# Kernel tuning notes

Measured on AMD Instinct MI355X. Metric: run time of the kernel, lower is better.

## Reference

```python
import jax, jax.numpy as jnp
import numpy as np


def setup_inputs() -> dict:
    key = jax.random.key(0)
    k1, k2 = jax.random.split(key)
    lut = jax.random.normal(k1, (1, 3, 33, 33, 33), dtype=jnp.float32)
    x = jax.random.uniform(k2, (8, 3, 1024, 1024), dtype=jnp.float32)
    return {"lut": lut, "x": x}


def reference(lut, x):
    # lut: [1, 3, D, D, D]; x: [B, 3, H, W] in [0,1]
    D = lut.shape[-1]
    lut0 = lut[0]  # [3, D, D, D], broadcast over batch (lut batch == 1)

    v = jnp.clip(x, 0.0, 1.0) * (D - 1)            # [B, 3, H, W]
    v = jnp.transpose(v, (0, 2, 3, 1))             # [B, H, W, 3]
    i0 = jnp.floor(v).astype(jnp.int32)            # [B, H, W, 3]
    i1 = jnp.minimum(i0 + 1, D - 1)
    f = v - i0.astype(v.dtype)                     # fractional part

    r0, g0, b0 = i0[..., 0], i0[..., 1], i0[..., 2]
    r1, g1, b1 = i1[..., 0], i1[..., 1], i1[..., 2]
    fr, fg, fb = f[..., 0], f[..., 1], f[..., 2]

    def gather(rr, gg, bb):
        # lut0[:, rr, gg, bb] -> [3, B, H, W] -> [B, 3, H, W]
        return jnp.transpose(lut0[:, rr, gg, bb], (1, 0, 2, 3))

    c000 = gather(r0, g0, b0)
    c100 = gather(r1, g0, b0)
    c010 = gather(r0, g1, b0)
    c110 = gather(r1, g1, b0)
    c001 = gather(r0, g0, b1)
    c101 = gather(r1, g0, b1)
    c011 = gather(r0, g1, b1)
    c111 = gather(r1, g1, b1)

    one = jnp.float32(1.0)
    w000 = ((one - fr) * (one - fg) * (one - fb))[:, None]
    w100 = (fr * (one - fg) * (one - fb))[:, None]
    w010 = ((one - fr) * fg * (one - fb))[:, None]
    w110 = (fr * fg * (one - fb))[:, None]
    w001 = ((one - fr) * (one - fg) * fb)[:, None]
    w101 = (fr * (one - fg) * fb)[:, None]
    w011 = ((one - fr) * fg * fb)[:, None]
    w111 = (fr * fg * fb)[:, None]

    out = (c000 * w000 + c100 * w100 + c010 * w010 + c110 * w110 +
           c001 * w001 + c101 * w101 + c011 * w011 + c111 * w111)
    return out  # [B, 3, H, W]
```

## Files before the change

### kernel.cpp

```cpp
#include <hip/hip_runtime.h>
#include <hip/hip_fp16.h>


#define D   33
#define D2  (33 * 33)
#define D3  (33 * 33 * 33)
#define HW  (1024 * 1024)
#define BATCH 8
#define QHW (HW / 4)
#define NG  (BATCH * QHW)
#define CHUNKS 256
#define GPC (NG / CHUNKS)
#define THREADS 1024

typedef float v4f __attribute__((ext_vector_type(4)));

__global__ __launch_bounds__(THREADS) void lut3d_kernel(
    const float* __restrict__ lut, const float* __restrict__ x,
    float* __restrict__ out)
{
    const int id    = blockIdx.x;
    const int xcd   = id & 7;
    const int slot  = id >> 3;
    const int c     = slot % 3;
    const int chunk = (slot / 3) * 8 + xcd;

    __shared__ __half2 ls[D3];
    {
        const float* lc = lut + c * D3;
        for (int i = threadIdx.x; i < D3; i += THREADS) {
            const int q  = i / D;
            const int b  = i - q * D;
            const float v0 = lc[i];
            const float v1 = (b < D - 1) ? lc[i + 1] : v0;
            ls[i] = __floats2half2_rn(v0, v1);
        }
    }
    __syncthreads();

    const int tid  = threadIdx.x;
    const int base = chunk * GPC;

    #pragma unroll 1
    for (int it = 0; it < GPC / THREADS; ++it) {
        const int g = base + it * THREADS + tid;
        const int b = g >> 18;
        const int p = (g & (QHW - 1)) * 4;

        const float* xb = x + (size_t)b * 3 * HW + p;
        const v4f xr = *(const v4f*)(xb);
        const v4f xg = *(const v4f*)(xb + HW);
        const v4f xB = *(const v4f*)(xb + 2 * HW);

        v4f oo;

        #pragma unroll
        for (int j = 0; j < 4; ++j) {
            const float vr = fminf(fmaxf(xr[j], 0.f), 1.f) * 32.f;
            const float vg = fminf(fmaxf(xg[j], 0.f), 1.f) * 32.f;
            const float vb = fminf(fmaxf(xB[j], 0.f), 1.f) * 32.f;

            const int r0 = min((int)vr, D - 2);
            const int g0 = min((int)vg, D - 2);
            const int b0 = min((int)vb, D - 2);
            const float fr = vr - (float)r0;
            const float fg = vg - (float)g0;
            const float fb = vb - (float)b0;

            const int idx = r0 * D2 + g0 * D + b0;

            const __half2 h00 = ls[idx];
            const __half2 h01 = ls[idx + D];
            const __half2 h10 = ls[idx + D2];
            const __half2 h11 = ls[idx + D2 + D];

            const float c00 = fmaf(fb, __high2float(h00) - __low2float(h00), __low2float(h00));
            const float c01 = fmaf(fb, __high2float(h01) - __low2float(h01), __low2float(h01));
            const float c10 = fmaf(fb, __high2float(h10) - __low2float(h10), __low2float(h10));
            const float c11 = fmaf(fb, __high2float(h11) - __low2float(h11), __low2float(h11));

            const float c0 = fmaf(fg, c01 - c00, c00);
            const float c1 = fmaf(fg, c11 - c10, c10);
            oo[j] = fmaf(fr, c1 - c0, c0);
        }

        float* ob = out + (size_t)b * 3 * HW + (size_t)c * HW + p;
        __builtin_nontemporal_store(oo, (v4f*)ob);
    }
}

extern "C" void kernel_launch(void* const* d_in, const int* in_sizes, int n_in,
                              void* d_out, int out_size, void* d_ws, size_t ws_size,
                              hipStream_t stream) {
    const float* lut = (const float*)d_in[0];
    const float* x   = (const float*)d_in[1];
    float* out = (float*)d_out;

    lut3d_kernel<<<dim3(3 * CHUNKS), THREADS, 0, stream>>>(lut, x, out);
}
```

Before: 224.4 us.

## Software-pipeline x loads and LDS gathers across fully unrolled iterations

Fully unrolls the per-block loop into a software pipeline. Input loads are issued two iterations ahead and the LDS gathers for the next group one iteration ahead, with a sched_barrier separating them from the current group's FMA and store. The LUT is stored as (value, delta) in half2, which saves one subtraction per corner. Batch and pointer setup is hoisted out of the loop and launch_bounds asks for more occupancy. The cost is higher register pressure, and storing the delta in fp16 may change rounding slightly.

```diff
diff --git a/kernel.cpp b/kernel.cpp
--- a/kernel.cpp
+++ b/kernel.cpp
@@ -6,16 +6,16 @@
 #define D2  (33 * 33)
 #define D3  (33 * 33 * 33)
 #define HW  (1024 * 1024)
-#define BATCH 8
 #define QHW (HW / 4)
-#define NG  (BATCH * QHW)
 #define CHUNKS 256
-#define GPC (NG / CHUNKS)
+#define GPC 8192
 #define THREADS 1024
+#define NIT (GPC / THREADS)
+#define STRIDE (THREADS * 4)
 
 typedef float v4f __attribute__((ext_vector_type(4)));
 
-__global__ __launch_bounds__(THREADS) void lut3d_kernel(
+__global__ __launch_bounds__(THREADS, 4) void lut3d_kernel(
     const float* __restrict__ lut, const float* __restrict__ x,
     float* __restrict__ out)
 {
@@ -30,63 +30,96 @@
         const float* lc = lut + c * D3;
         for (int i = threadIdx.x; i < D3; i += THREADS) {
             const int q  = i / D;
-            const int b  = i - q * D;
+            const int bb = i - q * D;
             const float v0 = lc[i];
-            const float v1 = (b < D - 1) ? lc[i + 1] : v0;
-            ls[i] = __floats2half2_rn(v0, v1);
+            const float v1 = (bb < D - 1) ? lc[i + 1] : v0;
+            ls[i] = __floats2half2_rn(v0, v1 - v0);
         }
     }
     __syncthreads();
 
-    const int tid  = threadIdx.x;
     const int base = chunk * GPC;
+    const int b    = base >> 18;
+    const float* __restrict__ xp = x + (size_t)b * 3 * HW;
+    float* __restrict__ op = out + (size_t)b * 3 * HW + (size_t)c * HW;
+    const int o0 = (base & (QHW - 1)) * 4 + threadIdx.x * 4;
 
-    #pragma unroll 1
-    for (int it = 0; it < GPC / THREADS; ++it) {
-        const int g = base + it * THREADS + tid;
-        const int b = g >> 18;
-        const int p = (g & (QHW - 1)) * 4;
+#define LOADX(o, R, G, B) do { \
+    (R) = *(const v4f*)(xp + (o)); \
+    (G) = *(const v4f*)(xp + HW + (o)); \
+    (B) = *(const v4f*)(xp + 2 * HW + (o)); } while (0)
 
-        const float* xb = x + (size_t)b * 3 * HW + p;
-        const v4f xr = *(const v4f*)(xb);
-        const v4f xg = *(const v4f*)(xb + HW);
-        const v4f xB = *(const v4f*)(xb + 2 * HW);
+#define PREP(XR, XG, XB, IDX, FR, FG, FB) do { \
+    _Pragma("unroll") \
+    for (int k = 0; k < 4; ++k) { \
+        const float vr = fminf(fmaxf((XR)[k], 0.f), 1.f) * 32.f; \
+        const float vg = fminf(fmaxf((XG)[k], 0.f), 1.f) * 32.f; \
+        const float vb = fminf(fmaxf((XB)[k], 0.f), 1.f) * 32.f; \
+        const int r0 = min((int)vr, D - 2); \
+        const int g0 = min((int)vg, D - 2); \
+        const int b0 = min((int)vb, D - 2); \
+        (FR)[k] = vr - (float)r0; \
+        (FG)[k] = vg - (float)g0; \
+        (FB)[k] = vb - (float)b0; \
+        (IDX)[k] = r0 * D2 + g0 * D + b0; } } while (0)
 
-        v4f oo;
+#define GATHER(IDX, H) do { \
+    _Pragma("unroll") \
+    for (int k = 0; k < 4; ++k) { \
+        const int idx = (IDX)[k]; \
+        (H)[k][0] = ls[idx]; \
+        (H)[k][1] = ls[idx + D]; \
+        (H)[k][2] = ls[idx + D2]; \
+        (H)[k][3] = ls[idx + D2 + D]; } } while (0)
 
+#define FMASTORE(o, FR, FG, FB, H) do { \
+    v4f oo; \
+    _Pragma("unroll") \
+    for (int k = 0; k < 4; ++k) { \
+        const float fb = (FB)[k], fg = (FG)[k], fr = (FR)[k]; \
+        const float c00 = fmaf(fb, __high2float((H)[k][0]), __low2float((H)[k][0])); \
+        const float c01 = fmaf(fb, __high2float((H)[k][1]), __low2float((H)[k][1])); \
+        const float c10 = fmaf(fb, __high2float((H)[k][2]), __low2float((H)[k][2])); \
+        const float c11 = fmaf(fb, __high2float((H)[k][3]), __low2float((H)[k][3])); \
+        const float c0 = fmaf(fg, c01 - c00, c00); \
+        const float c1 = fmaf(fg, c11 - c10, c10); \
+        oo[k] = fmaf(fr, c1 - c0, c0); } \
+    __builtin_nontemporal_store(oo, (v4f*)(op + (o))); } while (0)
+
+    v4f xr1, xg1, xb1;
+    int   idxA[4]; float frA[4], fgA[4], fbA[4]; __half2 hA[4][4];
+    {
+        v4f xr0, xg0, xb0;
+        LOADX(o0, xr0, xg0, xb0);
+        LOADX(o0 + STRIDE, xr1, xg1, xb1);
+        PREP(xr0, xg0, xb0, idxA, frA, fgA, fbA);
+        GATHER(idxA, hA);
+    }
+
+    #pragma unroll
+    for (int it = 0; it < NIT; ++it) {
+        v4f nxr, nxg, nxb;
+        if (it + 2 < NIT) LOADX(o0 + (it + 2) * STRIDE, nxr, nxg, nxb);
+        int idxN[4]; float frN[4], fgN[4], fbN[4]; __half2 hN[4][4];
+        if (it + 1 < NIT) {
+            PREP(xr1, xg1, xb1, idxN, frN, fgN, fbN);
+            GATHER(idxN, hN);
+        }
+        __builtin_amdgcn_sched_barrier(0);
+        FMASTORE(o0 + it * STRIDE, frA, fgA, fbA, hA);
+        xr1 = nxr; xg1 = nxg; xb1 = nxb;
         #pragma unroll
-        for (int j = 0; j < 4; ++j) {
-            const float vr = fminf(fmaxf(xr[j], 0.f), 1.f) * 32.f;
-            const float vg = fminf(fmaxf(xg[j], 0.f), 1.f) * 32.f;
-            const float vb = fminf(fmaxf(xB[j], 0.f), 1.f) * 32.f;
+        for (int k = 0; k < 4; ++k) {
+            idxA[k] = idxN[k]; frA[k] = frN[k]; fgA[k] = fgN[k]; fbA[k] = fbN[k];
+            hA[k][0] = hN[k][0]; hA[k][1] = hN[k][1];
+            hA[k][2] = hN[k][2]; hA[k][3] = hN[k][3];
+        }
+    }
 
-            const int r0 = min((int)vr, D - 2);
-            const int g0 = min((int)vg, D - 2);
-            const int b0 = min((int)vb, D - 2);
-            const float fr = vr - (float)r0;
-            const float fg = vg - (float)g0;
-            const float fb = vb - (float)b0;
-
-            const int idx = r0 * D2 + g0 * D + b0;
-
-            const __half2 h00 = ls[idx];
-            const __half2 h01 = ls[idx + D];
-            const __half2 h10 = ls[idx + D2];
-            const __half2 h11 = ls[idx + D2 + D];
-
-            const float c00 = fmaf(fb, __high2float(h00) - __low2float(h00), __low2float(h00));
-            const float c01 = fmaf(fb, __high2float(h01) - __low2float(h01), __low2float(h01));
-            const float c10 = fmaf(fb, __high2float(h10) - __low2float(h10), __low2float(h10));
-            const float c11 = fmaf(fb, __high2float(h11) - __low2float(h11), __low2float(h11));
-
-            const float c0 = fmaf(fg, c01 - c00, c00);
-            const float c1 = fmaf(fg, c11 - c10, c10);
-            oo[j] = fmaf(fr, c1 - c0, c0);
-        }
-
-        float* ob = out + (size_t)b * 3 * HW + (size_t)c * HW + p;
-        __builtin_nontemporal_store(oo, (v4f*)ob);
-    }
+#undef LOADX
+#undef PREP
+#undef GATHER
+#undef FMASTORE
 }
 
 extern "C" void kernel_launch(void* const* d_in, const int* in_sizes, int n_in,
```

Result: no change. 223.7 us (-0.3%).
